# Kernel optimization log

Hardware: AMD Instinct MI355X
Metric: run time of the kernel (lower is better)

Reference implementation:

```python
import jax, jax.numpy as jnp
import numpy as np

B, S, D = 4, 4096, 1024
DC = 1024  # d_chunk (defaults to d_model)
NUM_CLASSES = 4


def setup_inputs() -> dict:
    key = jax.random.key(0)
    ks = jax.random.split(key, 8)
    init = lambda k, shape: (jax.random.normal(k, shape, jnp.float32) * 0.02)
    return {
        "h": jax.random.normal(ks[0], (B, S, D), jnp.float32),
        "pseudo_labels": jax.random.randint(ks[1], (B, S), 0, NUM_CLASSES, jnp.int32),
        "Wl": init(ks[2], (D, NUM_CLASSES)), "bl": jnp.zeros((NUM_CLASSES,), jnp.float32),
        "Wq": init(ks[3], (D, DC)), "bq": jnp.zeros((DC,), jnp.float32),
        "Wk": init(ks[4], (D, DC)), "bk": jnp.zeros((DC,), jnp.float32),
        "Wv": init(ks[5], (D, D)), "bv": jnp.zeros((D,), jnp.float32),
        "Wo": init(ks[6], (D, D)), "bo": jnp.zeros((D,), jnp.float32),
    }


def _chunk_starts(labels):
    """BIOS chunking: label 0=B starts a chunk extended by following 1=I's;
    labels 1 (orphan I), 2=O, 3=S are singleton chunks. Returns bool [B,S]
    marking chunk starts. Parallel replacement for the torch while-loop."""
    def step(ext, lab):  # ext[b]: previous token can be extended by an I
        cont = (lab == 1) & ext          # this token continues prev chunk
        new_ext = (lab == 0) | cont      # B, or a continuing I, is extendable
        return new_ext, ~cont            # non-continuing token starts a chunk
    init = jnp.zeros(labels.shape[0], dtype=bool)
    _, starts_t = jax.lax.scan(step, init, labels.T)  # scan over seq axis
    return starts_t.T  # [B, S]


def reference(h, pseudo_labels, Wl, bl, Wq, bq, Wk, bk, Wv, bv, Wo, bo):
    b, s, d = h.shape
    dc = Wq.shape[1]

    logits = h @ Wl + bl                                  # [B,S,4]
    logp = jax.nn.log_softmax(logits, axis=-1)
    loss = -jnp.mean(jnp.take_along_axis(logp, pseudo_labels[..., None], axis=-1))

    pred = jnp.argmax(logits, axis=-1).astype(jnp.int32)  # [B,S]
    starts = _chunk_starts(pred)
    seg = jnp.cumsum(starts.astype(jnp.int32), axis=1) - 1  # segment id per token

    # Segment-mean pooling, padded to S possible chunks per batch element.
    seg_sum = jax.vmap(lambda x, ids: jax.ops.segment_sum(x, ids, num_segments=s))(h, seg)
    counts = jax.vmap(lambda ids: jax.ops.segment_sum(jnp.ones((s,), h.dtype), ids, num_segments=s))(seg)
    chunk_emb = seg_sum / jnp.maximum(counts, 1.0)[..., None]  # [B,S,D]
    valid = counts > 0                                         # [B,S]

    q = h @ Wq + bq              # [B,S,DC]
    k = chunk_emb @ Wk + bk      # [B,C,DC]
    v = chunk_emb @ Wv + bv      # [B,C,D]
    scale = jnp.asarray(1.0 / np.sqrt(dc), h.dtype)
    scores = jnp.einsum('bsd,bcd->bsc', q, k) * scale
    scores = jnp.where(valid[:, None, :], scores, jnp.asarray(-1e30, h.dtype))
    attn = jax.nn.softmax(scores, axis=-1)
    attended = jnp.einsum('bsc,bcd->bsd', attn, v)
    ch_out = attended @ Wo + bo
    return ch_out, loss
```

## Files before the change

kernel.cpp:

```cpp
#include <hip/hip_runtime.h>

typedef unsigned short u16;
typedef __attribute__((ext_vector_type(8))) short short8;
typedef __attribute__((ext_vector_type(8))) unsigned short ushort8;
typedef __attribute__((ext_vector_type(4))) unsigned short ushort4v;
typedef __attribute__((ext_vector_type(4))) float f32x4;

#define NB 4
#define SS 4096
#define DD 1024
#define CFENCE asm volatile("" ::: "memory")

__device__ __forceinline__ u16 f2bf(float x) {
  unsigned u = __builtin_bit_cast(unsigned, x);
  u = (u + 0x7FFFu + ((u >> 16) & 1u)) >> 16;
  return (u16)u;
}
__device__ __forceinline__ float bf2f(u16 b) {
  unsigned u = ((unsigned)b) << 16;
  return __builtin_bit_cast(float, u);
}
__device__ __forceinline__ void gload16(const void* g, void* l) {
  __builtin_amdgcn_global_load_lds((const __attribute__((address_space(1))) void*)g,
                                   (__attribute__((address_space(3))) void*)l, 16, 0, 0);
}
__device__ __forceinline__ int xcd_swz(int bid, int nwg) {
  const int x = bid & 7, idx = bid >> 3;
  const int q = nwg >> 3, r = nwg & 7;
  return (x < r ? x * (q + 1) : r * (q + 1) + (x - r) * q) + idx;
}

__global__ __launch_bounds__(256) void k_logits(
    const float* __restrict__ h, const int* __restrict__ lab,
    const float* __restrict__ Wl, const float* __restrict__ bl,
    u16* __restrict__ h16, int* __restrict__ pred, float* __restrict__ lossPart)
{
  const int t = threadIdx.x, w = t >> 6, lane = t & 63;
  const int tok = blockIdx.x * 4 + w;
  const float4* h4p = (const float4*)(h + (size_t)tok * DD);
  const float4* wl4 = (const float4*)Wl;
  float p0 = 0.f, p1 = 0.f, p2 = 0.f, p3 = 0.f;
#pragma unroll
  for (int i = 0; i < 4; ++i) {
    const int d = i * 256 + lane * 4;
    float4 hv = h4p[i * 64 + lane];
    ushort4v hb;
    hb[0] = f2bf(hv.x); hb[1] = f2bf(hv.y); hb[2] = f2bf(hv.z); hb[3] = f2bf(hv.w);
    *(ushort4v*)(h16 + (size_t)tok * DD + d) = hb;
    float4 w0 = wl4[d], w1 = wl4[d + 1], w2 = wl4[d + 2], w3 = wl4[d + 3];
    p0 += hv.x * w0.x + hv.y * w1.x + hv.z * w2.x + hv.w * w3.x;
    p1 += hv.x * w0.y + hv.y * w1.y + hv.z * w2.y + hv.w * w3.y;
    p2 += hv.x * w0.z + hv.y * w1.z + hv.z * w2.z + hv.w * w3.z;
    p3 += hv.x * w0.w + hv.y * w1.w + hv.z * w2.w + hv.w * w3.w;
  }
#pragma unroll
  for (int m = 32; m; m >>= 1) {
    p0 += __shfl_xor(p0, m); p1 += __shfl_xor(p1, m);
    p2 += __shfl_xor(p2, m); p3 += __shfl_xor(p3, m);
  }
  __shared__ float ls[4];
  if (lane == 0) {
    float l[4] = {p0 + bl[0], p1 + bl[1], p2 + bl[2], p3 + bl[3]};
    int bi = 0; float bv = l[0];
#pragma unroll
    for (int c = 1; c < 4; ++c) if (l[c] > bv) { bv = l[c]; bi = c; }
    pred[tok] = bi;
    float se = 0.f;
#pragma unroll
    for (int c = 0; c < 4; ++c) se += expf(l[c] - bv);
    float lse = bv + logf(se);
    ls[w] = lse - l[lab[tok]];
  }
  __syncthreads();
  if (t == 0) lossPart[blockIdx.x] = ls[0] + ls[1] + ls[2] + ls[3];
}

__global__ __launch_bounds__(256) void k_wconv(
    const float* __restrict__ W0, const float* __restrict__ W1,
    const float* __restrict__ W2, const float* __restrict__ W3,
    u16* __restrict__ Wt)
{
  const int gid = blockIdx.x * 256 + threadIdx.x;
  const int mat = gid >> 20;
  const int rem = gid & ((1 << 20) - 1);
  const int n = rem >> 10, k = rem & 1023;
  const float* W = (mat == 0) ? W0 : (mat == 1) ? W1 : (mat == 2) ? W2 : W3;
  const float v = (mat == 2) ? W[(size_t)n * 1024 + k] : W[(size_t)k * 1024 + n];
  Wt[(size_t)gid] = f2bf(v);
}

__global__ __launch_bounds__(256) void k_scan(
    const int* __restrict__ pred, int* __restrict__ cstart, int* __restrict__ ccnt)
{
  const int b = blockIdx.x, t = threadIdx.x;
  const int4* p4 = (const int4*)(pred + (size_t)b * SS);
  int labv[16];
#pragma unroll
  for (int i = 0; i < 4; ++i) {
    int4 v = p4[t * 4 + i];
    labv[i * 4 + 0] = v.x; labv[i * 4 + 1] = v.y;
    labv[i * 4 + 2] = v.z; labv[i * 4 + 3] = v.w;
  }
  int A = 0, Bc = 1;
#pragma unroll
  for (int e = 0; e < 16; ++e) {
    int a = (labv[e] == 0), bb = (labv[e] == 1);
    A = a | (bb & A);
    Bc = bb & Bc;
  }
  __shared__ int sA[256], sB[256], sC[256];
  sA[t] = A; sB[t] = Bc;
  __syncthreads();
  for (int off = 1; off < 256; off <<= 1) {
    int pa = 0, pb = 1;
    if (t >= off) { pa = sA[t - off]; pb = sB[t - off]; }
    __syncthreads();
    A = A | (Bc & pa); Bc = Bc & pb;
    sA[t] = A; sB[t] = Bc;
    __syncthreads();
  }
  const int extIn = (t == 0) ? 0 : sA[t - 1];
  int ext = extIn, nst = 0;
#pragma unroll
  for (int e = 0; e < 16; ++e) {
    int cont = (labv[e] == 1) & ext;
    nst += !cont;
    ext = (labv[e] == 0) | cont;
  }
  sC[t] = nst;
  __syncthreads();
  int tot = nst;
  for (int off = 1; off < 256; off <<= 1) {
    int pc = 0;
    if (t >= off) pc = sC[t - off];
    __syncthreads();
    tot += pc;
    sC[t] = tot;
    __syncthreads();
  }
  const int base = tot - nst;
  const int total = sC[255];
  if (t == 0) { ccnt[b] = total; cstart[b * (SS + 1) + total] = SS; }
  ext = extIn; int id = base;
#pragma unroll
  for (int e = 0; e < 16; ++e) {
    int cont = (labv[e] == 1) & ext;
    if (!cont) cstart[b * (SS + 1) + id++] = t * 16 + e;
    ext = (labv[e] == 0) | cont;
  }
}

__global__ __launch_bounds__(256) void k_pool(
    const float* __restrict__ h, const int* __restrict__ cstart,
    const int* __restrict__ ccnt, u16* __restrict__ cemb)
{
  const int t = threadIdx.x, w = t >> 6, lane = t & 63;
  const int gw = blockIdx.x * 4 + w;
  const int b = gw >> 12, c = gw & (SS - 1);
  u16* out = cemb + (size_t)gw * DD + lane * 16;
  if (c >= ccnt[b]) {
    ushort8 z = {0, 0, 0, 0, 0, 0, 0, 0};
    *(ushort8*)out = z; *(ushort8*)(out + 8) = z;
    return;
  }
  const int s0 = cstart[b * (SS + 1) + c], s1 = cstart[b * (SS + 1) + c + 1];
  float acc[16] = {};
  for (int s = s0; s < s1; ++s) {
    const float4* hp = (const float4*)(h + ((size_t)b * SS + s) * DD + lane * 16);
#pragma unroll
    for (int ii = 0; ii < 4; ++ii) {
      float4 v = hp[ii];
      acc[ii * 4 + 0] += v.x; acc[ii * 4 + 1] += v.y;
      acc[ii * 4 + 2] += v.z; acc[ii * 4 + 3] += v.w;
    }
  }
  const float inv = 1.f / (float)(s1 - s0);
  ushort8 o0, o1;
#pragma unroll
  for (int e = 0; e < 8; ++e) { o0[e] = f2bf(acc[e] * inv); o1[e] = f2bf(acc[8 + e] * inv); }
  *(ushort8*)out = o0; *(ushort8*)(out + 8) = o1;
}

__global__ __launch_bounds__(256) void k_bvwo(
    const float* __restrict__ bv, const float* __restrict__ Wo,
    const float* __restrict__ bo, float* __restrict__ outv)
{
  const int n = blockIdx.x * 256 + threadIdx.x;
  float s = 0.f;
#pragma unroll 8
  for (int j = 0; j < 1024; ++j) s += bv[j] * Wo[(size_t)j * 1024 + n];
  outv[n] = s;
}

__global__ __launch_bounds__(256) void k_wvo(
    const u16* __restrict__ WoT, const u16* __restrict__ Wvn, u16* __restrict__ WvoT)
{
  __shared__ u16 lA[64 * 64], lB[64 * 64];
  const int t = threadIdx.x, lane = t & 63, w = t >> 6;
  const int m0 = blockIdx.y * 64, n0 = blockIdx.x * 64;
  const int trow = t >> 3;
  const int schunk = ((t & 7) ^ (trow & 7)) * 8;
  const u16* Ag = WoT + (size_t)(m0 + trow) * 1024 + schunk;
  const u16* Bg = Wvn + (size_t)(n0 + trow) * 1024 + schunk;
  u16* dA = lA + t * 8;
  u16* dB = lB + t * 8;
  f32x4 acc[4];
#pragma unroll
  for (int i = 0; i < 4; ++i) acc[i] = (f32x4){0.f, 0.f, 0.f, 0.f};
  const int lrow = lane & 15, hi = lane >> 4;
  const int co0 = (hi ^ (lrow & 7)) * 8;
  const int co1 = ((4 + hi) ^ (lrow & 7)) * 8;
  for (int kt = 0; kt < 1024; kt += 64) {
    gload16(Ag + kt, dA); gload16(Ag + (size_t)32 * 1024 + kt, dA + 2048);
    gload16(Bg + kt, dB); gload16(Bg + (size_t)32 * 1024 + kt, dB + 2048);
    __syncthreads();
#pragma unroll
    for (int ks = 0; ks < 2; ++ks) {
      const int co = ks ? co1 : co0;
      short8 af = *(const short8*)(lA + (w * 16 + lrow) * 64 + co);
#pragma unroll
      for (int ni = 0; ni < 4; ++ni) {
        short8 bf8 = *(const short8*)(lB + (ni * 16 + lrow) * 64 + co);
        acc[ni] = __builtin_amdgcn_mfma_f32_16x16x32_bf16(af, bf8, acc[ni], 0, 0, 0);
      }
    }
    __syncthreads();
  }
#pragma unroll
  for (int ni = 0; ni < 4; ++ni)
#pragma unroll
    for (int q = 0; q < 4; ++q)
      WvoT[(size_t)(m0 + w * 16 + hi * 4 + q) * 1024 + n0 + ni * 16 + lrow] = f2bf(acc[ni][q]);
}

template <int OUTF32, int CLAMPK, int SKIPN>
__global__ __launch_bounds__(512, 2) void gemm256(
    const u16* __restrict__ A0p, const u16* __restrict__ A1p,
    const u16* __restrict__ A2p, const u16* __restrict__ A3p,
    const u16* __restrict__ A3bp,
    const u16* __restrict__ Bt, long strideB,
    void* __restrict__ C0, void* __restrict__ C1,
    void* __restrict__ C2, void* __restrict__ C3, void* __restrict__ C3b,
    const float* __restrict__ bias, float scale, int M, int N, int K,
    const int* __restrict__ ccnt, int zoff)
{
  __shared__ u16 lds[65536];
  u16* ldsA = lds;
  u16* ldsB = lds + 32768;
  const int t = threadIdx.x, lane = t & 63, w = t >> 6;
  const int wr = w >> 2, wc = w & 3;
  const int z = blockIdx.z + zoff;
  const int bid = blockIdx.y * gridDim.x + blockIdx.x;
  const int swz = xcd_swz(bid, gridDim.x * gridDim.y);
  const int m0 = (swz / gridDim.x) * 256, n0 = (swz % gridDim.x) * 256;

  int NT = K >> 6;
  if (SKIPN || CLAMPK) {
    const int cb = ccnt[z];
    const int ntc = (cb + 63) >> 6;
    if (SKIPN && n0 >= (ntc << 6)) return;
    if (CLAMPK && ntc < NT) NT = ntc;
  }

  const u16* A = (z == 0) ? A0p : (z == 1) ? A1p : (z == 2) ? A2p : A3p;
  void* Cp    = (z == 0) ? C0 : (z == 1) ? C1 : (z == 2) ? C2 : C3;
  int meffA = m0, meffC = m0;
  if (z == 3 && A3bp && m0 >= 2048) { A = A3bp; meffA = m0 - 2048; }
  if (z == 3 && C3b && m0 >= 2048) { Cp = C3b; meffC = m0 - 2048; }
  const u16* B = Bt + (size_t)z * strideB;

  f32x4 acc[8][4];
#pragma unroll
  for (int i = 0; i < 8; ++i)
#pragma unroll
    for (int j = 0; j < 4; ++j) acc[i][j] = (f32x4){0.f, 0.f, 0.f, 0.f};

  const int trow = t >> 3;
  const u16* Ag = A + (size_t)(meffA + trow) * K + ((t & 7) ^ (trow & 7)) * 8;
  const u16* Bg = B + (size_t)(n0 + trow) * K + ((t & 7) ^ (trow & 7)) * 8;
  u16* dA = ldsA + t * 8;
  u16* dB = ldsB + t * 8;

#define STG_AH0(BUF, KT) { gload16(Ag + (size_t)(KT),            dA + (BUF) * 16384 + 0 * 4096); \
                           gload16(Ag + (size_t)128 * K + (KT),  dA + (BUF) * 16384 + 2 * 4096); }
#define STG_AH1(BUF, KT) { gload16(Ag + (size_t)64 * K + (KT),   dA + (BUF) * 16384 + 1 * 4096); \
                           gload16(Ag + (size_t)192 * K + (KT),  dA + (BUF) * 16384 + 3 * 4096); }
#define STG_B(BUF, KT)   { gload16(Bg + (size_t)(KT),            dB + (BUF) * 16384 + 0 * 4096); \
                           gload16(Bg + (size_t)64 * K + (KT),   dB + (BUF) * 16384 + 1 * 4096); \
                           gload16(Bg + (size_t)128 * K + (KT),  dB + (BUF) * 16384 + 2 * 4096); \
                           gload16(Bg + (size_t)192 * K + (KT),  dB + (BUF) * 16384 + 3 * 4096); }
#define RD_A(BASE, ROFF) \
  { _Pragma("unroll") for (int mi = 0; mi < 4; ++mi) { \
      af[mi][0] = *(const short8*)((BASE) + (wr * 128 + (ROFF) + mi * 16 + lrow) * 64 + co0); \
      af[mi][1] = *(const short8*)((BASE) + (wr * 128 + (ROFF) + mi * 16 + lrow) * 64 + co1); } }
#define RD_B(BASE) \
  { _Pragma("unroll") for (int ni = 0; ni < 4; ++ni) { \
      bf[ni][0] = *(const short8*)((BASE) + (wc * 64 + ni * 16 + lrow) * 64 + co0); \
      bf[ni][1] = *(const short8*)((BASE) + (wc * 64 + ni * 16 + lrow) * 64 + co1); } }
#define MFMA32(MH) \
  { _Pragma("unroll") for (int ks = 0; ks < 2; ++ks) \
    _Pragma("unroll") for (int mi = 0; mi < 4; ++mi) \
      _Pragma("unroll") for (int ni = 0; ni < 4; ++ni) \
        acc[(MH) * 4 + mi][ni] = __builtin_amdgcn_mfma_f32_16x16x32_bf16( \
            af[mi][ks], bf[ni][ks], acc[(MH) * 4 + mi][ni], 0, 0, 0); }

  const int lrow = lane & 15, hi = lane >> 4;
  const int co0 = (hi ^ (lrow & 7)) * 8;
  const int co1 = ((4 + hi) ^ (lrow & 7)) * 8;

  STG_AH0(0, 0); STG_AH1(0, 0); STG_B(0, 0);
  if (NT > 1) {
    STG_AH0(1, 64); STG_B(1, 64);
    asm volatile("s_waitcnt vmcnt(6)" ::: "memory");
  } else {
    asm volatile("s_waitcnt vmcnt(0)" ::: "memory");
  }
  __builtin_amdgcn_s_barrier();
  CFENCE;

  short8 af[4][2], bf[4][2];
  for (int j = 0; j < NT; ++j) {
    const int cur = j & 1;
    const u16* bufA = ldsA + cur * 16384;
    const u16* bufB = ldsB + cur * 16384;
    RD_A(bufA, 0);
    RD_B(bufB);
    if (j + 1 < NT) STG_AH1(cur ^ 1, (j + 1) << 6);
    CFENCE;
    __builtin_amdgcn_s_barrier();
    __builtin_amdgcn_s_setprio(1);
    MFMA32(0);
    __builtin_amdgcn_s_setprio(0);
    __builtin_amdgcn_sched_barrier(0);
    __builtin_amdgcn_s_barrier();
    CFENCE;
    RD_A(bufA, 64);
    if (j + 2 < NT) { STG_AH0(cur, (j + 2) << 6); STG_B(cur, (j + 2) << 6); }
    CFENCE;
    __builtin_amdgcn_s_barrier();
    __builtin_amdgcn_s_setprio(1);
    MFMA32(1);
    __builtin_amdgcn_s_setprio(0);
    if (j + 2 < NT)       asm volatile("s_waitcnt vmcnt(6)" ::: "memory");
    else if (j + 2 == NT) asm volatile("s_waitcnt vmcnt(0)" ::: "memory");
    __builtin_amdgcn_sched_barrier(0);
    __builtin_amdgcn_s_barrier();
    CFENCE;
  }

  if (OUTF32) {
    const int rowb = m0 + wr * 128 + (lane >> 4) * 4;
#pragma unroll
    for (int n = 0; n < 4; ++n) {
      const int col = n0 + wc * 64 + n * 16 + (lane & 15);
      const float bv = bias ? bias[col] : 0.f;
#pragma unroll
      for (int m = 0; m < 8; ++m)
#pragma unroll
        for (int q = 0; q < 4; ++q)
          ((float*)Cp)[(size_t)(rowb + m * 16 + q) * N + col] = acc[m][n][q] * scale + bv;
    }
  } else {
    __syncthreads();
    u16* cls = lds;
    const int rowl = wr * 128 + (lane >> 4) * 4;
#pragma unroll
    for (int n = 0; n < 4; ++n) {
      const int coll = wc * 64 + n * 16 + (lane & 15);
      const float bv = bias ? bias[n0 + coll] : 0.f;
#pragma unroll
      for (int m = 0; m < 8; ++m)
#pragma unroll
        for (int q = 0; q < 4; ++q)
          cls[(rowl + m * 16 + q) * 256 + coll] = f2bf(acc[m][n][q] * scale + bv);
    }
    __syncthreads();
    u16* Cu = (u16*)Cp;
#pragma unroll
    for (int ps = 0; ps < 16; ++ps) {
      const int f = ps * 512 + t;
      const int row = f >> 5, col8 = (f & 31) * 8;
      *(ushort8*)(Cu + (size_t)(meffC + row) * N + n0 + col8) =
          *(const ushort8*)(cls + row * 256 + col8);
    }
  }
#undef STG_AH0
#undef STG_AH1
#undef STG_B
#undef RD_A
#undef RD_B
#undef MFMA32
}

__global__ __launch_bounds__(256) void k_softmax(
    u16* __restrict__ s0, u16* __restrict__ s1, u16* __restrict__ s2,
    u16* __restrict__ s3a, u16* __restrict__ s3b, const int* __restrict__ ccnt)
{
  const int t = threadIdx.x, lane = t & 63, w = t >> 6;
  const int row = blockIdx.x, b = blockIdx.y;
  u16* sc;
  if (b == 0) sc = s0 + (size_t)row * SS;
  else if (b == 1) sc = s1 + (size_t)row * SS;
  else if (b == 2) sc = s2 + (size_t)row * SS;
  else sc = (row < 2048) ? s3a + (size_t)row * SS : s3b + (size_t)(row - 2048) * SS;
  const int Cb = ccnt[b];
  u16* p = sc + t * 16;
  ushort8 v0 = *(ushort8*)p, v1 = *(ushort8*)(p + 8);
  float x[16];
#pragma unroll
  for (int e = 0; e < 8; ++e) { x[e] = bf2f(v0[e]); x[8 + e] = bf2f(v1[e]); }
  const int cb0 = t * 16;
  float m = -1e30f;
#pragma unroll
  for (int e = 0; e < 16; ++e) if (cb0 + e < Cb) m = fmaxf(m, x[e]);
#pragma unroll
  for (int off = 32; off; off >>= 1) m = fmaxf(m, __shfl_xor(m, off));
  __shared__ float red[4], red2[4];
  if (lane == 0) red[w] = m;
  __syncthreads();
  m = fmaxf(fmaxf(red[0], red[1]), fmaxf(red[2], red[3]));
  float ssum = 0.f;
#pragma unroll
  for (int e = 0; e < 16; ++e) {
    float ev = (cb0 + e < Cb) ? __expf(x[e] - m) : 0.f;
    x[e] = ev; ssum += ev;
  }
#pragma unroll
  for (int off = 32; off; off >>= 1) ssum += __shfl_xor(ssum, off);
  if (lane == 0) red2[w] = ssum;
  __syncthreads();
  ssum = red2[0] + red2[1] + red2[2] + red2[3];
  const float inv = 1.f / ssum;
#pragma unroll
  for (int e = 0; e < 8; ++e) { v0[e] = f2bf(x[e] * inv); v1[e] = f2bf(x[8 + e] * inv); }
  *(ushort8*)p = v0; *(ushort8*)(p + 8) = v1;
}

__global__ __launch_bounds__(256) void k_transpose(
    const u16* __restrict__ v, u16* __restrict__ vt)
{
  __shared__ u16 ts[64][80];
  const int t = threadIdx.x;
  const int d0 = blockIdx.x * 64, c0 = blockIdx.y * 64, b = blockIdx.z;
#pragma unroll
  for (int p = 0; p < 2; ++p) {
    const int idx = p * 256 + t, r = idx >> 3, cc = idx & 7;
    ushort8 val = *(const ushort8*)(v + ((size_t)b * SS + c0 + r) * DD + d0 + cc * 8);
    *(ushort8*)&ts[r][cc * 8] = val;
  }
  __syncthreads();
#pragma unroll
  for (int p = 0; p < 2; ++p) {
    const int idx = p * 256 + t, r = idx >> 3, cc = idx & 7;
    ushort8 o;
#pragma unroll
    for (int e = 0; e < 8; ++e) o[e] = ts[cc * 8 + e][r];
    *(ushort8*)(vt + ((size_t)b * DD + d0 + r) * SS + c0 + cc * 8) = o;
  }
}

__global__ __launch_bounds__(256) void k_lossfin(
    const float* __restrict__ part, float* __restrict__ out)
{
  const int t = threadIdx.x, lane = t & 63, w = t >> 6;
  float s = 0.f;
  for (int i = t; i < 4096; i += 256) s += part[i];
#pragma unroll
  for (int off = 32; off; off >>= 1) s += __shfl_xor(s, off);
  __shared__ float r[4];
  if (lane == 0) r[w] = s;
  __syncthreads();
  if (t == 0) out[0] = (r[0] + r[1] + r[2] + r[3]) * (1.f / (NB * SS));
}

extern "C" void kernel_launch(void* const* d_in, const int* in_sizes, int n_in,
                              void* d_out, int out_size, void* d_ws, size_t ws_size,
                              hipStream_t stream) {
  const float* h  = (const float*)d_in[0];
  const int* plab = (const int*)d_in[1];
  const float* Wl = (const float*)d_in[2];
  const float* bl = (const float*)d_in[3];
  const float* Wq = (const float*)d_in[4];
  const float* bq = (const float*)d_in[5];
  const float* Wk = (const float*)d_in[6];
  const float* bk = (const float*)d_in[7];
  const float* Wv = (const float*)d_in[8];
  const float* bv = (const float*)d_in[9];
  const float* Wo = (const float*)d_in[10];
  const float* bo = (const float*)d_in[11];
  float* out = (float*)d_out;

  char* ws = (char*)d_ws;
  const size_t SZ = (size_t)NB * SS * DD * 2;
  const size_t SD = (size_t)SS * DD;
  u16* h16      = (u16*)(ws + 0 * SZ);
  u16* cemb     = (u16*)(ws + 1 * SZ);
  u16* q        = (u16*)(ws + 2 * SZ);
  u16* kk       = (u16*)(ws + 3 * SZ);
  u16* vv       = (u16*)(ws + 4 * SZ);
  u16* vt       = (u16*)(ws + 5 * SZ);
  u16* Wt       = (u16*)(ws + 6 * SZ);
  char* ws2     = ws + 6 * SZ + (size_t)4 * 1024 * 1024 * 2;
  int* pred     = (int*)ws2;
  int* cstart   = (int*)(ws2 + 65536);
  int* ccnt     = (int*)(ws2 + 65536 + 4 * (SS + 1) * 4);
  float* lossPart = (float*)(ws2 + 65536 + 4 * (SS + 1) * 4 + 64);
  float* bvwo   = (float*)(ws2 + 65536 + 4 * (SS + 1) * 4 + 64 + 16384);
  u16* s0 = h16;
  u16* s1 = cemb;
  u16* s2 = vv;
  u16* s3a = q;
  u16* s3b = kk;

  k_logits<<<dim3(NB * SS / 4), 256, 0, stream>>>(h, plab, Wl, bl, h16, pred, lossPart);
  k_wconv<<<dim3(4 * 1024 * 1024 / 256), 256, 0, stream>>>(Wq, Wk, Wv, Wo, Wt);
  k_scan<<<dim3(NB), 256, 0, stream>>>(pred, cstart, ccnt);
  k_pool<<<dim3(NB * SS / 4), 256, 0, stream>>>(h, cstart, ccnt, cemb);
  k_bvwo<<<dim3(4), 256, 0, stream>>>(bv, Wo, bo, bvwo);

  gemm256<0, 0, 0><<<dim3(DD / 256, NB * SS / 256, 1), 512, 0, stream>>>(
      h16, h16, h16, h16, nullptr, Wt, 0, q, q, q, q, nullptr,
      bq, 1.f, NB * SS, DD, DD, nullptr, 0);
  k_wvo<<<dim3(16, 16), 256, 0, stream>>>(Wt + 3 * (1 << 20), Wt + 2 * (1 << 20), Wt);
  gemm256<0, 0, 0><<<dim3(DD / 256, NB * SS / 256, 1), 512, 0, stream>>>(
      cemb, cemb, cemb, cemb, nullptr, Wt + (1 << 20), 0, kk, kk, kk, kk, nullptr,
      bk, 1.f, NB * SS, DD, DD, nullptr, 0);
  gemm256<0, 0, 0><<<dim3(DD / 256, NB * SS / 256, 1), 512, 0, stream>>>(
      cemb, cemb, cemb, cemb, nullptr, Wt, 0, vv, vv, vv, vv, nullptr,
      bvwo, 1.f, NB * SS, DD, DD, nullptr, 0);
  k_transpose<<<dim3(DD / 64, SS / 64, NB), 256, 0, stream>>>(vv, vt);

  const float scl = 1.f / 32.f;
  gemm256<0, 0, 1><<<dim3(SS / 256, SS / 256, 3), 512, 0, stream>>>(
      q, q + SD, q + 2 * SD, nullptr, nullptr, kk, (long)SD,
      s0, s1, s2, nullptr, nullptr, nullptr, scl, SS, SS, DD, ccnt, 0);
  gemm256<0, 0, 1><<<dim3(SS / 256, SS / 256, 1), 512, 0, stream>>>(
      q, q, q, q + 3 * SD, nullptr, kk, (long)SD,
      nullptr, nullptr, nullptr, s3a, s3b, nullptr, scl, SS, SS, DD, ccnt, 3);
  k_softmax<<<dim3(SS, NB), 256, 0, stream>>>(s0, s1, s2, s3a, s3b, ccnt);
  gemm256<1, 1, 0><<<dim3(DD / 256, SS / 256, NB), 512, 0, stream>>>(
      s0, s1, s2, s3a, s3b, vt, (long)SD,
      out, out + SD, out + 2 * SD, out + 3 * SD, nullptr,
      bo, 1.f, SS, DD, SS, ccnt, 0);
  k_lossfin<<<dim3(1), 256, 0, stream>>>(lossPart, out + (size_t)NB * SS * DD);
}
```

Baseline: 559.0 us.

## Skip padded chunk rows in K/V GEMMs, softmax, transpose; pool from bf16

Measured after the change: 555.7 us. Within noise of the previous version (-0.6%).

```diff
diff --git a/kernel.cpp b/kernel.cpp
--- a/kernel.cpp
+++ b/kernel.cpp
@@ -151,7 +151,7 @@
 }
 
 __global__ __launch_bounds__(256) void k_pool(
-    const float* __restrict__ h, const int* __restrict__ cstart,
+    const u16* __restrict__ h16, const int* __restrict__ cstart,
     const int* __restrict__ ccnt, u16* __restrict__ cemb)
 {
   const int t = threadIdx.x, w = t >> 6, lane = t & 63;
@@ -166,13 +166,10 @@
   const int s0 = cstart[b * (SS + 1) + c], s1 = cstart[b * (SS + 1) + c + 1];
   float acc[16] = {};
   for (int s = s0; s < s1; ++s) {
-    const float4* hp = (const float4*)(h + ((size_t)b * SS + s) * DD + lane * 16);
-#pragma unroll
-    for (int ii = 0; ii < 4; ++ii) {
-      float4 v = hp[ii];
-      acc[ii * 4 + 0] += v.x; acc[ii * 4 + 1] += v.y;
-      acc[ii * 4 + 2] += v.z; acc[ii * 4 + 3] += v.w;
-    }
+    const ushort8* hp = (const ushort8*)(h16 + ((size_t)b * SS + s) * DD + lane * 16);
+    ushort8 a = hp[0], bb = hp[1];
+#pragma unroll
+    for (int e = 0; e < 8; ++e) { acc[e] += bf2f(a[e]); acc[8 + e] += bf2f(bb[e]); }
   }
   const float inv = 1.f / (float)(s1 - s0);
   ushort8 o0, o1;
@@ -233,7 +230,7 @@
       WvoT[(size_t)(m0 + w * 16 + hi * 4 + q) * 1024 + n0 + ni * 16 + lrow] = f2bf(acc[ni][q]);
 }
 
-template <int OUTF32, int CLAMPK, int SKIPN>
+template <int OUTF32, int CLAMPK, int SKIPN, int CLAMPM>
 __global__ __launch_bounds__(512, 2) void gemm256(
     const u16* __restrict__ A0p, const u16* __restrict__ A1p,
     const u16* __restrict__ A2p, const u16* __restrict__ A3p,
@@ -260,6 +257,11 @@
     const int ntc = (cb + 63) >> 6;
     if (SKIPN && n0 >= (ntc << 6)) return;
     if (CLAMPK && ntc < NT) NT = ntc;
+  }
+  if (CLAMPM) {
+    const int bb = m0 >> 12;
+    const int ntc64 = ((ccnt[bb] + 63) >> 6) << 6;
+    if ((m0 & 4095) >= ntc64) return;
   }
 
   const u16* A = (z == 0) ? A0p : (z == 1) ? A1p : (z == 2) ? A2p : A3p;
@@ -303,6 +305,32 @@
       _Pragma("unroll") for (int ni = 0; ni < 4; ++ni) \
         acc[(MH) * 4 + mi][ni] = __builtin_amdgcn_mfma_f32_16x16x32_bf16( \
             af[mi][ks], bf[ni][ks], acc[(MH) * 4 + mi][ni], 0, 0, 0); }
+#define KSTEP(BUF, JV) { \
+    const u16* bufA = ldsA + (BUF) * 16384; \
+    const u16* bufB = ldsB + (BUF) * 16384; \
+    RD_A(bufA, 0); \
+    RD_B(bufB); \
+    if ((JV) + 1 < NT) STG_AH1((BUF) ^ 1, ((JV) + 1) << 6); \
+    CFENCE; \
+    __builtin_amdgcn_s_barrier(); \
+    __builtin_amdgcn_s_setprio(1); \
+    MFMA32(0); \
+    __builtin_amdgcn_s_setprio(0); \
+    __builtin_amdgcn_sched_barrier(0); \
+    __builtin_amdgcn_s_barrier(); \
+    CFENCE; \
+    RD_A(bufA, 64); \
+    if ((JV) + 2 < NT) { STG_AH0((BUF), ((JV) + 2) << 6); STG_B((BUF), ((JV) + 2) << 6); } \
+    CFENCE; \
+    __builtin_amdgcn_s_barrier(); \
+    __builtin_amdgcn_s_setprio(1); \
+    MFMA32(1); \
+    __builtin_amdgcn_s_setprio(0); \
+    if ((JV) + 2 < NT)       asm volatile("s_waitcnt vmcnt(6)" ::: "memory"); \
+    else if ((JV) + 2 == NT) asm volatile("s_waitcnt vmcnt(0)" ::: "memory"); \
+    __builtin_amdgcn_sched_barrier(0); \
+    __builtin_amdgcn_s_barrier(); \
+    CFENCE; }
 
   const int lrow = lane & 15, hi = lane >> 4;
   const int co0 = (hi ^ (lrow & 7)) * 8;
@@ -319,34 +347,9 @@
   CFENCE;
 
   short8 af[4][2], bf[4][2];
-  for (int j = 0; j < NT; ++j) {
-    const int cur = j & 1;
-    const u16* bufA = ldsA + cur * 16384;
-    const u16* bufB = ldsB + cur * 16384;
-    RD_A(bufA, 0);
-    RD_B(bufB);
-    if (j + 1 < NT) STG_AH1(cur ^ 1, (j + 1) << 6);
-    CFENCE;
-    __builtin_amdgcn_s_barrier();
-    __builtin_amdgcn_s_setprio(1);
-    MFMA32(0);
-    __builtin_amdgcn_s_setprio(0);
-    __builtin_amdgcn_sched_barrier(0);
-    __builtin_amdgcn_s_barrier();
-    CFENCE;
-    RD_A(bufA, 64);
-    if (j + 2 < NT) { STG_AH0(cur, (j + 2) << 6); STG_B(cur, (j + 2) << 6); }
-    CFENCE;
-    __builtin_amdgcn_s_barrier();
-    __builtin_amdgcn_s_setprio(1);
-    MFMA32(1);
-    __builtin_amdgcn_s_setprio(0);
-    if (j + 2 < NT)       asm volatile("s_waitcnt vmcnt(6)" ::: "memory");
-    else if (j + 2 == NT) asm volatile("s_waitcnt vmcnt(0)" ::: "memory");
-    __builtin_amdgcn_sched_barrier(0);
-    __builtin_amdgcn_s_barrier();
-    CFENCE;
-  }
+  int j = 0;
+  for (; j + 2 <= NT; j += 2) { KSTEP(0, j); KSTEP(1, j + 1); }
+  if (j < NT) KSTEP(0, j);
 
   if (OUTF32) {
     const int rowb = m0 + wr * 128 + (lane >> 4) * 4;
@@ -390,6 +393,7 @@
 #undef RD_A
 #undef RD_B
 #undef MFMA32
+#undef KSTEP
 }
 
 __global__ __launch_bounds__(256) void k_softmax(
@@ -404,12 +408,15 @@
   else if (b == 2) sc = s2 + (size_t)row * SS;
   else sc = (row < 2048) ? s3a + (size_t)row * SS : s3b + (size_t)(row - 2048) * SS;
   const int Cb = ccnt[b];
-  u16* p = sc + t * 16;
-  ushort8 v0 = *(ushort8*)p, v1 = *(ushort8*)(p + 8);
+  const int ntc64 = ((Cb + 63) >> 6) << 6;
+  const int cb0 = t * 16;
+  const int active = cb0 < ntc64;
+  u16* p = sc + cb0;
+  ushort8 v0 = {0, 0, 0, 0, 0, 0, 0, 0}, v1 = {0, 0, 0, 0, 0, 0, 0, 0};
+  if (active) { v0 = *(ushort8*)p; v1 = *(ushort8*)(p + 8); }
   float x[16];
 #pragma unroll
   for (int e = 0; e < 8; ++e) { x[e] = bf2f(v0[e]); x[8 + e] = bf2f(v1[e]); }
-  const int cb0 = t * 16;
   float m = -1e30f;
 #pragma unroll
   for (int e = 0; e < 16; ++e) if (cb0 + e < Cb) m = fmaxf(m, x[e]);
@@ -431,22 +438,27 @@
   __syncthreads();
   ssum = red2[0] + red2[1] + red2[2] + red2[3];
   const float inv = 1.f / ssum;
-#pragma unroll
-  for (int e = 0; e < 8; ++e) { v0[e] = f2bf(x[e] * inv); v1[e] = f2bf(x[8 + e] * inv); }
-  *(ushort8*)p = v0; *(ushort8*)(p + 8) = v1;
+  if (active) {
+#pragma unroll
+    for (int e = 0; e < 8; ++e) { v0[e] = f2bf(x[e] * inv); v1[e] = f2bf(x[8 + e] * inv); }
+    *(ushort8*)p = v0; *(ushort8*)(p + 8) = v1;
+  }
 }
 
 __global__ __launch_bounds__(256) void k_transpose(
-    const u16* __restrict__ v, u16* __restrict__ vt)
-{
+    const u16* __restrict__ v, u16* __restrict__ vt, const int* __restrict__ ccnt)
+{
+  const int b = blockIdx.z;
+  const int c0 = blockIdx.y * 64;
+  if (c0 >= (((ccnt[b] + 63) >> 6) << 6)) return;
   __shared__ u16 ts[64][80];
   const int t = threadIdx.x;
-  const int d0 = blockIdx.x * 64, c0 = blockIdx.y * 64, b = blockIdx.z;
+  const int d0 = blockIdx.x * 64;
 #pragma unroll
   for (int p = 0; p < 2; ++p) {
     const int idx = p * 256 + t, r = idx >> 3, cc = idx & 7;
     ushort8 val = *(const ushort8*)(v + ((size_t)b * SS + c0 + r) * DD + d0 + cc * 8);
-    *(ushort8*)&ts[r][cc * 8] = val;
+    *(ushort8*)&ts[r][(cc ^ ((r >> 3) & 7)) * 8] = val;
   }
   __syncthreads();
 #pragma unroll
@@ -454,7 +466,8 @@
     const int idx = p * 256 + t, r = idx >> 3, cc = idx & 7;
     ushort8 o;
 #pragma unroll
-    for (int e = 0; e < 8; ++e) o[e] = ts[cc * 8 + e][r];
+    for (int e = 0; e < 8; ++e)
+      o[e] = ts[cc * 8 + e][(((r >> 3) ^ cc) << 3) + (r & 7)];
     *(ushort8*)(vt + ((size_t)b * DD + d0 + r) * SS + c0 + cc * 8) = o;
   }
 }
@@ -515,30 +528,30 @@
   k_logits<<<dim3(NB * SS / 4), 256, 0, stream>>>(h, plab, Wl, bl, h16, pred, lossPart);
   k_wconv<<<dim3(4 * 1024 * 1024 / 256), 256, 0, stream>>>(Wq, Wk, Wv, Wo, Wt);
   k_scan<<<dim3(NB), 256, 0, stream>>>(pred, cstart, ccnt);
-  k_pool<<<dim3(NB * SS / 4), 256, 0, stream>>>(h, cstart, ccnt, cemb);
+  k_pool<<<dim3(NB * SS / 4), 256, 0, stream>>>(h16, cstart, ccnt, cemb);
   k_bvwo<<<dim3(4), 256, 0, stream>>>(bv, Wo, bo, bvwo);
 
-  gemm256<0, 0, 0><<<dim3(DD / 256, NB * SS / 256, 1), 512, 0, stream>>>(
+  gemm256<0, 0, 0, 0><<<dim3(DD / 256, NB * SS / 256, 1), 512, 0, stream>>>(
       h16, h16, h16, h16, nullptr, Wt, 0, q, q, q, q, nullptr,
       bq, 1.f, NB * SS, DD, DD, nullptr, 0);
   k_wvo<<<dim3(16, 16), 256, 0, stream>>>(Wt + 3 * (1 << 20), Wt + 2 * (1 << 20), Wt);
-  gemm256<0, 0, 0><<<dim3(DD / 256, NB * SS / 256, 1), 512, 0, stream>>>(
+  gemm256<0, 0, 0, 1><<<dim3(DD / 256, NB * SS / 256, 1), 512, 0, stream>>>(
       cemb, cemb, cemb, cemb, nullptr, Wt + (1 << 20), 0, kk, kk, kk, kk, nullptr,
-      bk, 1.f, NB * SS, DD, DD, nullptr, 0);
-  gemm256<0, 0, 0><<<dim3(DD / 256, NB * SS / 256, 1), 512, 0, stream>>>(
+      bk, 1.f, NB * SS, DD, DD, ccnt, 0);
+  gemm256<0, 0, 0, 1><<<dim3(DD / 256, NB * SS / 256, 1), 512, 0, stream>>>(
       cemb, cemb, cemb, cemb, nullptr, Wt, 0, vv, vv, vv, vv, nullptr,
-      bvwo, 1.f, NB * SS, DD, DD, nullptr, 0);
-  k_transpose<<<dim3(DD / 64, SS / 64, NB), 256, 0, stream>>>(vv, vt);
+      bvwo, 1.f, NB * SS, DD, DD, ccnt, 0);
+  k_transpose<<<dim3(DD / 64, SS / 64, NB), 256, 0, stream>>>(vv, vt, ccnt);
 
   const float scl = 1.f / 32.f;
-  gemm256<0, 0, 1><<<dim3(SS / 256, SS / 256, 3), 512, 0, stream>>>(
+  gemm256<0, 0, 1, 0><<<dim3(SS / 256, SS / 256, 3), 512, 0, stream>>>(
       q, q + SD, q + 2 * SD, nullptr, nullptr, kk, (long)SD,
       s0, s1, s2, nullptr, nullptr, nullptr, scl, SS, SS, DD, ccnt, 0);
-  gemm256<0, 0, 1><<<dim3(SS / 256, SS / 256, 1), 512, 0, stream>>>(
+  gemm256<0, 0, 1, 0><<<dim3(SS / 256, SS / 256, 1), 512, 0, stream>>>(
       q, q, q, q + 3 * SD, nullptr, kk, (long)SD,
       nullptr, nullptr, nullptr, s3a, s3b, nullptr, scl, SS, SS, DD, ccnt, 3);
   k_softmax<<<dim3(SS, NB), 256, 0, stream>>>(s0, s1, s2, s3a, s3b, ccnt);
-  gemm256<1, 1, 0><<<dim3(DD / 256, SS / 256, NB), 512, 0, stream>>>(
+  gemm256<1, 1, 0, 0><<<dim3(DD / 256, SS / 256, NB), 512, 0, stream>>>(
       s0, s1, s2, s3a, s3b, vt, (long)SD,
       out, out + SD, out + 2 * SD, out + 3 * SD, nullptr,
       bo, 1.f, SS, DD, SS, ccnt, 0);
```
